# Performance work log

Hardware: AMD Instinct MI355X
Metric: run time of the kernel (lower is better)

The kernel has to match this reference:

```python
import jax, jax.numpy as jnp
import numpy as np

BS, C, N, L = 2, 64, 400, 12   # [bs, c, N, L]
D, H = 128, 8                  # model_dim, num_heads
HD = D // H                    # head_dim = 16
FF = 1024                      # feed_forward_dim
EPS_LN = 1e-5
EPS_NORM = 1e-12


def setup_inputs() -> dict:
    key = jax.random.key(0)
    ks = jax.random.split(key, 24)
    w = lambda k, shape: jax.random.normal(k, shape, jnp.float32) * 0.02
    inp = {
        "x":     jax.random.normal(ks[0], (BS, C, N, L), jnp.float32),
        "x_au1": jax.random.normal(ks[1], (BS, C, N, L), jnp.float32),
        "x_au2": jax.random.normal(ks[2], (BS, C, N, L), jnp.float32),
        # projections stored as [in, out] so y = x @ W + b
        "WQ1": w(ks[3], (C, D)),  "bQ1": jnp.zeros((D,)),
        "WQ2": w(ks[4], (C, D)),  "bQ2": jnp.zeros((D,)),
        "WK1": w(ks[5], (C, D)),  "bK1": jnp.zeros((D,)),
        "WK2": w(ks[6], (C, D)),  "bK2": jnp.zeros((D,)),
        "WV":  w(ks[7], (C, D)),  "bV":  jnp.zeros((D,)),
        "Wo":  w(ks[8], (D, C)),  "bo":  jnp.zeros((C,)),
        "Wf1": w(ks[9], (C, FF)), "bf1": jnp.zeros((FF,)),
        "Wf2": w(ks[10], (FF, C)),"bf2": jnp.zeros((C,)),
        "g1": jnp.ones((C,)), "be1": jnp.zeros((C,)),
        "g2": jnp.ones((C,)), "be2": jnp.zeros((C,)),
        "temperature": jnp.ones((H,)),
        "alphas": jnp.ones((2,)) / 2.0,
    }
    return inp


def _layernorm(x, g, b):
    m = jnp.mean(x, axis=-1, keepdims=True)
    v = jnp.var(x, axis=-1, keepdims=True)
    return (x - m) * jax.lax.rsqrt(v + EPS_LN) * g + b


def _l2norm(x):
    n = jnp.linalg.norm(x, axis=-1, keepdims=True)
    return x / jnp.maximum(n, EPS_NORM)


def _topk_masked(attn, k):
    # keep entries >= k-th largest along last axis (ties measure-zero for floats)
    kth = jax.lax.top_k(attn, k)[0][..., -1:]
    return jnp.where(attn >= kth, attn, -jnp.inf)


def reference(x, x_au1, x_au2, WQ1, bQ1, WQ2, bQ2, WK1, bK1, WK2, bK2,
              WV, bV, Wo, bo, Wf1, bf1, Wf2, bf2, g1, be1, g2, be2,
              temperature, alphas):
    # [bs,c,N,L] -> [bs,L,N,c]
    xt  = jnp.transpose(x,     (0, 3, 2, 1))
    a1t = jnp.transpose(x_au1, (0, 3, 2, 1))
    a2t = jnp.transpose(x_au2, (0, 3, 2, 1))
    bs, Lq, Nq, c = xt.shape

    def heads(t):  # [bs,L,N,D] -> [bs,L,N,H,hd]
        return t.reshape(bs, Lq, Nq, H, HD)

    q1 = _l2norm(heads(a1t @ WQ1 + bQ1))
    q2 = _l2norm(heads(a2t @ WQ2 + bQ2))
    k1 = _l2norm(heads(xt  @ WK1 + bK1))
    k2 = _l2norm(heads(xt  @ WK2 + bK2))
    v  = heads(xt @ WV + bV)

    # dual cosine attention scores: [bs,H,L,N,N]
    attn = (jnp.einsum('blnhd,blmhd->bhlnm', q1, k1)
            + jnp.einsum('blnhd,blmhd->bhlnm', q2, k2))
    attn = attn * temperature.reshape(1, H, 1, 1, 1)

    k_top1 = max(1, Nq // 2)
    k_top2 = max(1, Nq // 4)
    p1 = jax.nn.softmax(_topk_masked(attn, k_top1), axis=-1)
    p2 = jax.nn.softmax(_topk_masked(attn, k_top2), axis=-1)

    out1 = jnp.einsum('bhlnm,blmhd->blnhd', p1, v)
    out2 = jnp.einsum('bhlnm,blmhd->blnhd', p2, v)
    al = jax.nn.softmax(alphas)
    out = (out1 * al[0] + out2 * al[1]).reshape(bs, Lq, Nq, D)

    out = out @ Wo + bo
    out = _layernorm(xt + out, g1, be1)
    ff = jax.nn.relu(out @ Wf1 + bf1) @ Wf2 + bf2
    out = _layernorm(out + ff, g2, be2)
    out = jnp.transpose(out, (0, 3, 2, 1))  # back to [bs,c,N,L]

    attn_flat = attn.reshape(bs * H, Lq, Nq, Nq)
    p2_flat = p2.reshape(bs * H, Lq, Nq, Nq)
    return out, attn_flat, p2_flat
```

## Files before the change

### kernel.cpp

```cpp
#include <hip/hip_runtime.h>
#include <math.h>

#define BSZ 2
#define CHN 64
#define NPT 400
#define LW  12
#define DM  128
#define NH  8
#define HDM 16
#define FFD 1024
#define NTOK (BSZ*LW*NPT)

#define TA 16
__global__ __launch_bounds__(128) void stage_a(
    const float* __restrict__ x, const float* __restrict__ xa1, const float* __restrict__ xa2,
    const float* __restrict__ WQ1, const float* __restrict__ bQ1,
    const float* __restrict__ WQ2, const float* __restrict__ bQ2,
    const float* __restrict__ WK1, const float* __restrict__ bK1,
    const float* __restrict__ WK2, const float* __restrict__ bK2,
    const float* __restrict__ WV,  const float* __restrict__ bV,
    float* __restrict__ q1n, float* __restrict__ q2n,
    float* __restrict__ k1n, float* __restrict__ k2n, float* __restrict__ vv)
{
  __shared__ float xv[TA][CHN], a1v[TA][CHN], a2v[TA][CHN];
  const int tid = threadIdx.x;
  const int t0 = blockIdx.x * TA;
  for (int i = tid; i < TA*CHN; i += 128) {
    int tt = i & (TA-1), c = i >> 4;
    int token = t0 + tt;
    int n = token % NPT; int bl = token / NPT; int l = bl % LW; int b = bl / LW;
    int gidx = ((b*CHN + c)*NPT + n)*LW + l;
    xv[tt][c] = x[gidx]; a1v[tt][c] = xa1[gidx]; a2v[tt][c] = xa2[gidx];
  }
  __syncthreads();
  const int d = tid;
  float aq1[TA], aq2[TA], ak1[TA], ak2[TA], av[TA];
  float b1 = bQ1[d], b2 = bQ2[d], b3 = bK1[d], b4 = bK2[d], b5 = bV[d];
  #pragma unroll
  for (int t = 0; t < TA; ++t) { aq1[t]=b1; aq2[t]=b2; ak1[t]=b3; ak2[t]=b4; av[t]=b5; }
  for (int c = 0; c < CHN; ++c) {
    float w1 = WQ1[c*DM + d], w2 = WQ2[c*DM + d], w3 = WK1[c*DM + d],
          w4 = WK2[c*DM + d], w5 = WV[c*DM + d];
    #pragma unroll
    for (int t = 0; t < TA; ++t) {
      float xc = xv[t][c], x1 = a1v[t][c], x2 = a2v[t][c];
      aq1[t] += x1*w1; aq2[t] += x2*w2; ak1[t] += xc*w3; ak2[t] += xc*w4; av[t] += xc*w5;
    }
  }
  const int h = d >> 4, dd = d & 15;
  #pragma unroll
  for (int t = 0; t < TA; ++t) {
    float s1 = aq1[t]*aq1[t], s2 = aq2[t]*aq2[t], s3 = ak1[t]*ak1[t], s4 = ak2[t]*ak2[t];
    #pragma unroll
    for (int m = 1; m < 16; m <<= 1) {
      s1 += __shfl_xor(s1, m); s2 += __shfl_xor(s2, m);
      s3 += __shfl_xor(s3, m); s4 += __shfl_xor(s4, m);
    }
    float i1 = 1.f/fmaxf(sqrtf(s1),1e-12f), i2 = 1.f/fmaxf(sqrtf(s2),1e-12f),
          i3 = 1.f/fmaxf(sqrtf(s3),1e-12f), i4 = 1.f/fmaxf(sqrtf(s4),1e-12f);
    int token = t0 + t;
    int n = token % NPT; int bl = token / NPT; int l = bl % LW; int b = bl / LW;
    int base = (((b*LW + l)*NH + h)*NPT + n)*HDM + dd;
    q1n[base] = aq1[t]*i1; q2n[base] = aq2[t]*i2;
    k1n[base] = ak1[t]*i3; k2n[base] = ak2[t]*i4; vv[base] = av[t];
  }
}

__device__ __forceinline__ unsigned okey(float xf) {
  unsigned u = __float_as_uint(xf);
  return (u & 0x80000000u) ? ~u : (u | 0x80000000u);
}

__global__ __launch_bounds__(256, 2) void stage_b(
    const float* __restrict__ q1n, const float* __restrict__ q2n,
    const float* __restrict__ k1n, const float* __restrict__ k2n,
    const float* __restrict__ vv,
    const float* __restrict__ temperature, const float* __restrict__ alphas,
    float* __restrict__ attn_o, float* __restrict__ p2_o, float* __restrict__ oa)
{
  __shared__ float4 k1s[4*401], k2s[4*401], vs[4*401];
  int wg = blockIdx.x;
  const int s = wg & 3; wg >>= 2;
  const int l = wg % LW; wg /= LW;
  const int h = wg & 7; const int b = wg >> 3;
  const int tid = threadIdx.x, lane = tid & 63, wave = tid >> 6;

  const int slice = (b*LW + l)*NH + h;
  const int oslice = (b*NH + h)*LW + l;
  const float4* k1g = (const float4*)(k1n + slice*NPT*HDM);
  const float4* k2g = (const float4*)(k2n + slice*NPT*HDM);
  const float4* vg  = (const float4*)(vv  + slice*NPT*HDM);
  for (int i = tid; i < NPT*4; i += 256) {
    int m = i >> 2, w4 = i & 3;
    k1s[w4*401 + m] = k1g[i];
    k2s[w4*401 + m] = k2g[i];
    vs [w4*401 + m] = vg[i];
  }
  __syncthreads();

  const float temp = temperature[h];
  float a0 = alphas[0], a1 = alphas[1];
  float amx = fmaxf(a0, a1);
  float e0 = __expf(a0 - amx), e1 = __expf(a1 - amx);
  float al0 = e0/(e0+e1), al1 = e1/(e0+e1);

  const float* q1base = q1n + slice*NPT*HDM;
  const float* q2base = q2n + slice*NPT*HDM;
  float* attn_base = attn_o + (size_t)oslice*NPT*NPT;
  float* p2_base   = p2_o   + (size_t)oslice*NPT*NPT;
  const int tokbase = (b*LW + l)*NPT;

  for (int bi = wave; bi < 25; bi += 4) {
    const int nb = s*100 + bi*4;
    float sc[4][7];
    #pragma unroll
    for (int r = 0; r < 4; ++r)
      #pragma unroll
      for (int j = 0; j < 7; ++j) sc[r][j] = 0.f;

    #pragma unroll
    for (int ch = 0; ch < 4; ++ch) {
      float4 q1c[4], q2c[4];
      #pragma unroll
      for (int r = 0; r < 4; ++r) {
        q1c[r] = *(const float4*)(q1base + (nb+r)*HDM + ch*4);
        q2c[r] = *(const float4*)(q2base + (nb+r)*HDM + ch*4);
      }
      #pragma unroll
      for (int j = 0; j < 7; ++j) {
        int m = lane + 64*j;
        if (j < 6 || lane < 16) {
          float4 kc1 = k1s[ch*401 + m];
          float4 kc2 = k2s[ch*401 + m];
          #pragma unroll
          for (int r = 0; r < 4; ++r) {
            sc[r][j] += q1c[r].x*kc1.x + q1c[r].y*kc1.y + q1c[r].z*kc1.z + q1c[r].w*kc1.w
                      + q2c[r].x*kc2.x + q2c[r].y*kc2.y + q2c[r].z*kc2.z + q2c[r].w*kc2.w;
          }
        }
      }
    }
    #pragma unroll
    for (int r = 0; r < 4; ++r) {
      #pragma unroll
      for (int j = 0; j < 7; ++j) {
        sc[r][j] *= temp;
        int m = lane + 64*j;
        if (j < 6 || lane < 16)
          __builtin_nontemporal_store(sc[r][j], &attn_base[(nb + r)*NPT + m]);
      }
    }
    #pragma unroll
    for (int r = 0; r < 4; ++r) {
      unsigned key[7];
      #pragma unroll
      for (int j = 0; j < 7; ++j) {
        bool valid = (j < 6) || (lane < 16);
        key[j] = valid ? okey(sc[r][j]) : 0u;
      }
      float am = -3.4e38f;
      #pragma unroll
      for (int j = 0; j < 7; ++j) if ((j < 6) || (lane < 16)) am = fmaxf(am, sc[r][j]);
      #pragma unroll
      for (int m2 = 1; m2 < 64; m2 <<= 1) am = fmaxf(am, __shfl_xor(am, m2));

      unsigned v1 = 0u, v2 = 0u;
      bool d1 = false, d2 = false;
      #pragma clang loop unroll(disable)
      for (int bit = 31; bit >= 0; --bit) {
        if (!d1) {
          unsigned T1 = v1 | (1u << bit);
          int c1 = 0;
          #pragma unroll
          for (int j = 0; j < 7; ++j) c1 += __popcll(__ballot(key[j] >= T1));
          if (c1 >= 200) { v1 = T1; if (c1 == 200) d1 = true; }
        }
        if (!d2) {
          unsigned T2 = v2 | (1u << bit);
          int c2 = 0;
          #pragma unroll
          for (int j = 0; j < 7; ++j) c2 += __popcll(__ballot(key[j] >= T2));
          if (c2 >= 100) { v2 = T2; if (c2 == 100) d2 = true; }
        }
        if (d1 && d2) break;
      }

      float e[7]; float s1 = 0.f, s2 = 0.f;
      #pragma unroll
      for (int j = 0; j < 7; ++j) {
        e[j] = ((j < 6) || (lane < 16)) ? __expf(sc[r][j] - am) : 0.f;
        s1 += (key[j] >= v1) ? e[j] : 0.f;
        s2 += (key[j] >= v2) ? e[j] : 0.f;
      }
      #pragma unroll
      for (int m2 = 1; m2 < 64; m2 <<= 1) { s1 += __shfl_xor(s1, m2); s2 += __shfl_xor(s2, m2); }
      float rz1 = 1.f / s1, rz2 = 1.f / s2;
      float c1 = al0 * rz1, c2 = al1 * rz2;
      #pragma unroll
      for (int j = 0; j < 7; ++j) {
        int m = lane + 64*j;
        float p2v = (key[j] >= v2) ? e[j]*rz2 : 0.f;
        if ((j < 6) || (lane < 16))
          __builtin_nontemporal_store(p2v, &p2_base[(nb + r)*NPT + m]);
        sc[r][j] = e[j] * (((key[j] >= v1) ? c1 : 0.f) + ((key[j] >= v2) ? c2 : 0.f));
      }
    }
    #pragma unroll
    for (int half = 0; half < 2; ++half) {
      float buf[32];
      #pragma unroll
      for (int i = 0; i < 32; ++i) buf[i] = 0.f;
      #pragma unroll
      for (int j = 0; j < 7; ++j) {
        int m = lane + 64*j;
        if (j < 6 || lane < 16) {
          float4 w0 = vs[(half*2+0)*401 + m];
          float4 w1 = vs[(half*2+1)*401 + m];
          #pragma unroll
          for (int r = 0; r < 4; ++r) {
            float wr = sc[r][j];
            buf[r*8+0] += wr*w0.x; buf[r*8+1] += wr*w0.y;
            buf[r*8+2] += wr*w0.z; buf[r*8+3] += wr*w0.w;
            buf[r*8+4] += wr*w1.x; buf[r*8+5] += wr*w1.y;
            buf[r*8+6] += wr*w1.z; buf[r*8+7] += wr*w1.w;
          }
        }
      }
      #pragma unroll
      for (int st = 0; st < 5; ++st) {
        int bsel = (lane >> st) & 1;
        #pragma unroll
        for (int u = 0; u < (32 >> (st+1)); ++u) {
          float lo = buf[2*u], hi = buf[2*u+1];
          float keep = bsel ? hi : lo;
          float send = bsel ? lo : hi;
          float recv = __shfl_xor(send, 1 << st);
          buf[u] = keep + recv;
        }
      }
      float res = buf[0] + __shfl_xor(buf[0], 32);
      if (lane < 32) {
        int rr = lane >> 3, dlo = lane & 7;
        oa[(tokbase + nb + rr)*DM + h*HDM + half*8 + dlo] = res;
      }
    }
  }
}

#define TC 32
__global__ __launch_bounds__(256, 2) void stage_c(
    const float* __restrict__ oa, const float* __restrict__ x,
    const float* __restrict__ Wo, const float* __restrict__ bo,
    const float* __restrict__ Wf1, const float* __restrict__ bf1,
    const float* __restrict__ Wf2, const float* __restrict__ bf2,
    const float* __restrict__ g1, const float* __restrict__ be1,
    const float* __restrict__ g2, const float* __restrict__ be2,
    float* __restrict__ outp)
{
  __shared__ float4 oa_lds[TC*32];
  __shared__ float4 y1_lds[TC*16];
  __shared__ float4 act_lds[TC*64];
  const int tid = threadIdx.x;
  const int t0 = blockIdx.x * TC;
  const float4* oag = (const float4*)(oa + t0*DM);
  for (int i = tid; i < TC*32; i += 256) oa_lds[i] = oag[i];
  __syncthreads();

  const int c = tid & 63, g = tid >> 6;
  float bo_c = bo[c], g1c = g1[c], be1c = be1[c], g2c = g2[c], be2c = be2[c], bf2c = bf2[c];

  float o1[8];
  #pragma unroll
  for (int k = 0; k < 8; ++k) o1[k] = bo_c;
  for (int d4 = 0; d4 < 32; ++d4) {
    float w0 = Wo[(4*d4+0)*CHN + c];
    float w1 = Wo[(4*d4+1)*CHN + c];
    float w2 = Wo[(4*d4+2)*CHN + c];
    float w3 = Wo[(4*d4+3)*CHN + c];
    #pragma unroll
    for (int k = 0; k < 8; ++k) {
      float4 u = oa_lds[(g + 4*k)*32 + d4];
      o1[k] += u.x*w0 + u.y*w1 + u.z*w2 + u.w*w3;
    }
  }
  float y1r[8];
  #pragma unroll
  for (int k = 0; k < 8; ++k) {
    int token = t0 + g + 4*k;
    int n = token % NPT; int bl = token / NPT; int l = bl % LW; int b = bl / LW;
    float val = o1[k] + x[((b*CHN + c)*NPT + n)*LW + l];
    float sm = val, sq = val*val;
    #pragma unroll
    for (int m2 = 1; m2 < 64; m2 <<= 1) { sm += __shfl_xor(sm, m2); sq += __shfl_xor(sq, m2); }
    float mean = sm * (1.f/64.f);
    float var = sq * (1.f/64.f) - mean*mean;
    float y = (val - mean) * rsqrtf(var + 1e-5f) * g1c + be1c;
    y1r[k] = y;
    ((float*)y1_lds)[(g + 4*k)*CHN + c] = y;
  }
  __syncthreads();

  float o2a[8];
  #pragma unroll
  for (int k = 0; k < 8; ++k) o2a[k] = 0.f;

  for (int fb = 0; fb < 4; ++fb) {
    {
      const int ft = tid & 63, ga = tid >> 6;
      const int f = fb*256 + ft*4;
      float4 facc[8];
      float4 bb = *(const float4*)(bf1 + f);
      #pragma unroll
      for (int k = 0; k < 8; ++k) facc[k] = bb;
      for (int c4 = 0; c4 < 16; ++c4) {
        float4 w0 = *(const float4*)(Wf1 + (4*c4+0)*FFD + f);
        float4 w1 = *(const float4*)(Wf1 + (4*c4+1)*FFD + f);
        float4 w2 = *(const float4*)(Wf1 + (4*c4+2)*FFD + f);
        float4 w3 = *(const float4*)(Wf1 + (4*c4+3)*FFD + f);
        #pragma unroll
        for (int k = 0; k < 8; ++k) {
          float4 y4 = y1_lds[(ga + 4*k)*16 + c4];
          facc[k].x += y4.x*w0.x + y4.y*w1.x + y4.z*w2.x + y4.w*w3.x;
          facc[k].y += y4.x*w0.y + y4.y*w1.y + y4.z*w2.y + y4.w*w3.y;
          facc[k].z += y4.x*w0.z + y4.y*w1.z + y4.z*w2.z + y4.w*w3.z;
          facc[k].w += y4.x*w0.w + y4.y*w1.w + y4.z*w2.w + y4.w*w3.w;
        }
      }
      #pragma unroll
      for (int k = 0; k < 8; ++k) {
        float4 rv;
        rv.x = fmaxf(facc[k].x, 0.f); rv.y = fmaxf(facc[k].y, 0.f);
        rv.z = fmaxf(facc[k].z, 0.f); rv.w = fmaxf(facc[k].w, 0.f);
        act_lds[(ga + 4*k)*64 + ft] = rv;
      }
    }
    __syncthreads();
    for (int f4 = 0; f4 < 64; ++f4) {
      int f = fb*256 + f4*4;
      float w0 = Wf2[(f+0)*CHN + c];
      float w1 = Wf2[(f+1)*CHN + c];
      float w2 = Wf2[(f+2)*CHN + c];
      float w3 = Wf2[(f+3)*CHN + c];
      #pragma unroll
      for (int k = 0; k < 8; ++k) {
        float4 a4 = act_lds[(g + 4*k)*64 + f4];
        o2a[k] += a4.x*w0 + a4.y*w1 + a4.z*w2 + a4.w*w3;
      }
    }
    __syncthreads();
  }
  #pragma unroll
  for (int k = 0; k < 8; ++k) {
    int token = t0 + g + 4*k;
    int n = token % NPT; int bl = token / NPT; int l = bl % LW; int b = bl / LW;
    float val = y1r[k] + o2a[k] + bf2c;
    float sm = val, sq = val*val;
    #pragma unroll
    for (int m2 = 1; m2 < 64; m2 <<= 1) { sm += __shfl_xor(sm, m2); sq += __shfl_xor(sq, m2); }
    float mean = sm * (1.f/64.f);
    float var = sq * (1.f/64.f) - mean*mean;
    float y = (val - mean) * rsqrtf(var + 1e-5f) * g2c + be2c;
    outp[((b*CHN + c)*NPT + n)*LW + l] = y;
  }
}

extern "C" void kernel_launch(void* const* d_in, const int* in_sizes, int n_in,
                              void* d_out, int out_size, void* d_ws, size_t ws_size,
                              hipStream_t stream) {
  const float* x    = (const float*)d_in[0];
  const float* xa1  = (const float*)d_in[1];
  const float* xa2  = (const float*)d_in[2];
  const float* WQ1  = (const float*)d_in[3];
  const float* bQ1  = (const float*)d_in[4];
  const float* WQ2  = (const float*)d_in[5];
  const float* bQ2  = (const float*)d_in[6];
  const float* WK1  = (const float*)d_in[7];
  const float* bK1  = (const float*)d_in[8];
  const float* WK2  = (const float*)d_in[9];
  const float* bK2  = (const float*)d_in[10];
  const float* WV   = (const float*)d_in[11];
  const float* bV   = (const float*)d_in[12];
  const float* Wo   = (const float*)d_in[13];
  const float* bo   = (const float*)d_in[14];
  const float* Wf1  = (const float*)d_in[15];
  const float* bf1  = (const float*)d_in[16];
  const float* Wf2  = (const float*)d_in[17];
  const float* bf2  = (const float*)d_in[18];
  const float* g1   = (const float*)d_in[19];
  const float* be1  = (const float*)d_in[20];
  const float* g2   = (const float*)d_in[21];
  const float* be2  = (const float*)d_in[22];
  const float* temp = (const float*)d_in[23];
  const float* alph = (const float*)d_in[24];

  float* outp   = (float*)d_out;
  float* attn_o = outp + (size_t)BSZ*CHN*NPT*LW;
  float* p2_o   = attn_o + (size_t)BSZ*NH*LW*NPT*NPT;

  const size_t SLICE = (size_t)BSZ*LW*NH*NPT*HDM;
  float* w   = (float*)d_ws;
  float* q1n = w;             w += SLICE;
  float* q2n = w;             w += SLICE;
  float* k1n = w;             w += SLICE;
  float* k2n = w;             w += SLICE;
  float* vv  = w;             w += SLICE;
  float* oa  = w;             w += (size_t)NTOK*DM;

  stage_a<<<NTOK/TA, 128, 0, stream>>>(x, xa1, xa2, WQ1, bQ1, WQ2, bQ2,
                                       WK1, bK1, WK2, bK2, WV, bV,
                                       q1n, q2n, k1n, k2n, vv);
  stage_b<<<BSZ*NH*LW*4, 256, 0, stream>>>(q1n, q2n, k1n, k2n, vv,
                                           temp, alph, attn_o, p2_o, oa);
  stage_c<<<NTOK/TC, 256, 0, stream>>>(oa, x, Wo, bo, Wf1, bf1, Wf2, bf2,
                                       g1, be1, g2, be2, outp);
}
```

Before: 1.338 ms.

## Split attention rows over more workgroups and interleave per-row top-k bisection

Stage_b now splits each (b,l,h) slice into 8 workgroups instead of 4, using an uneven 13/12 row-group split. This doubles the grid to fill more compute units, at the cost of loading K/V into shared memory twice as often. The radix-bisection top-k threshold search now runs over all 4 rows of a block inside one bit loop, so the serial ballot chains from different rows overlap and there is more instruction-level parallelism. The price is more registers for the key arrays, which could hurt occupancy.

```diff
diff --git a/kernel.cpp b/kernel.cpp
--- a/kernel.cpp
+++ b/kernel.cpp
@@ -10,6 +10,7 @@
 #define HDM 16
 #define FFD 1024
 #define NTOK (BSZ*LW*NPT)
+#define SPLIT 8
 
 #define TA 16
 __global__ __launch_bounds__(128) void stage_a(
@@ -80,10 +81,13 @@
 {
   __shared__ float4 k1s[4*401], k2s[4*401], vs[4*401];
   int wg = blockIdx.x;
-  const int s = wg & 3; wg >>= 2;
+  const int s = wg & (SPLIT-1); wg /= SPLIT;
   const int l = wg % LW; wg /= LW;
   const int h = wg & 7; const int b = wg >> 3;
   const int tid = threadIdx.x, lane = tid & 63, wave = tid >> 6;
+
+  const int g0  = s*12 + (s < 4 ? s : 4);
+  const int cnt = (s < 4) ? 13 : 12;
 
   const int slice = (b*LW + l)*NH + h;
   const int oslice = (b*NH + h)*LW + l;
@@ -110,8 +114,8 @@
   float* p2_base   = p2_o   + (size_t)oslice*NPT*NPT;
   const int tokbase = (b*LW + l)*NPT;
 
-  for (int bi = wave; bi < 25; bi += 4) {
-    const int nb = s*100 + bi*4;
+  for (int bi = wave; bi < cnt; bi += 4) {
+    const int nb = (g0 + bi)*4;
     float sc[4][7];
     #pragma unroll
     for (int r = 0; r < 4; ++r)
@@ -150,47 +154,58 @@
           __builtin_nontemporal_store(sc[r][j], &attn_base[(nb + r)*NPT + m]);
       }
     }
+    unsigned key[4][7];
+    #pragma unroll
+    for (int r = 0; r < 4; ++r)
+      #pragma unroll
+      for (int j = 0; j < 7; ++j) {
+        bool valid = (j < 6) || (lane < 16);
+        key[r][j] = valid ? okey(sc[r][j]) : 0u;
+      }
+    float am[4];
     #pragma unroll
     for (int r = 0; r < 4; ++r) {
-      unsigned key[7];
-      #pragma unroll
-      for (int j = 0; j < 7; ++j) {
-        bool valid = (j < 6) || (lane < 16);
-        key[j] = valid ? okey(sc[r][j]) : 0u;
-      }
-      float am = -3.4e38f;
-      #pragma unroll
-      for (int j = 0; j < 7; ++j) if ((j < 6) || (lane < 16)) am = fmaxf(am, sc[r][j]);
-      #pragma unroll
-      for (int m2 = 1; m2 < 64; m2 <<= 1) am = fmaxf(am, __shfl_xor(am, m2));
-
-      unsigned v1 = 0u, v2 = 0u;
-      bool d1 = false, d2 = false;
-      #pragma clang loop unroll(disable)
-      for (int bit = 31; bit >= 0; --bit) {
-        if (!d1) {
-          unsigned T1 = v1 | (1u << bit);
-          int c1 = 0;
+      float a = -3.4e38f;
+      #pragma unroll
+      for (int j = 0; j < 7; ++j) if ((j < 6) || (lane < 16)) a = fmaxf(a, sc[r][j]);
+      am[r] = a;
+    }
+    #pragma unroll
+    for (int m2 = 1; m2 < 64; m2 <<= 1) {
+      #pragma unroll
+      for (int r = 0; r < 4; ++r) am[r] = fmaxf(am[r], __shfl_xor(am[r], m2));
+    }
+    unsigned v1[4] = {0u,0u,0u,0u}, v2[4] = {0u,0u,0u,0u};
+    unsigned done = 0u;
+    #pragma clang loop unroll(disable)
+    for (int bit = 31; bit >= 0; --bit) {
+      #pragma unroll
+      for (int r = 0; r < 4; ++r) {
+        if (!(done & (1u << r))) {
+          unsigned T = v1[r] | (1u << bit);
+          int c = 0;
           #pragma unroll
-          for (int j = 0; j < 7; ++j) c1 += __popcll(__ballot(key[j] >= T1));
-          if (c1 >= 200) { v1 = T1; if (c1 == 200) d1 = true; }
-        }
-        if (!d2) {
-          unsigned T2 = v2 | (1u << bit);
-          int c2 = 0;
+          for (int j = 0; j < 7; ++j) c += __popcll(__ballot(key[r][j] >= T));
+          if (c >= 200) { v1[r] = T; if (c == 200) done |= (1u << r); }
+        }
+        if (!(done & (16u << r))) {
+          unsigned T = v2[r] | (1u << bit);
+          int c = 0;
           #pragma unroll
-          for (int j = 0; j < 7; ++j) c2 += __popcll(__ballot(key[j] >= T2));
-          if (c2 >= 100) { v2 = T2; if (c2 == 100) d2 = true; }
-        }
-        if (d1 && d2) break;
-      }
-
+          for (int j = 0; j < 7; ++j) c += __popcll(__ballot(key[r][j] >= T));
+          if (c >= 100) { v2[r] = T; if (c == 100) done |= (16u << r); }
+        }
+      }
+      if (done == 0xFFu) break;
+    }
+    #pragma unroll
+    for (int r = 0; r < 4; ++r) {
       float e[7]; float s1 = 0.f, s2 = 0.f;
       #pragma unroll
       for (int j = 0; j < 7; ++j) {
-        e[j] = ((j < 6) || (lane < 16)) ? __expf(sc[r][j] - am) : 0.f;
-        s1 += (key[j] >= v1) ? e[j] : 0.f;
-        s2 += (key[j] >= v2) ? e[j] : 0.f;
+        e[j] = ((j < 6) || (lane < 16)) ? __expf(sc[r][j] - am[r]) : 0.f;
+        s1 += (key[r][j] >= v1[r]) ? e[j] : 0.f;
+        s2 += (key[r][j] >= v2[r]) ? e[j] : 0.f;
       }
       #pragma unroll
       for (int m2 = 1; m2 < 64; m2 <<= 1) { s1 += __shfl_xor(s1, m2); s2 += __shfl_xor(s2, m2); }
@@ -199,10 +214,10 @@
       #pragma unroll
       for (int j = 0; j < 7; ++j) {
         int m = lane + 64*j;
-        float p2v = (key[j] >= v2) ? e[j]*rz2 : 0.f;
+        float p2v = (key[r][j] >= v2[r]) ? e[j]*rz2 : 0.f;
         if ((j < 6) || (lane < 16))
           __builtin_nontemporal_store(p2v, &p2_base[(nb + r)*NPT + m]);
-        sc[r][j] = e[j] * (((key[j] >= v1) ? c1 : 0.f) + ((key[j] >= v2) ? c2 : 0.f));
+        sc[r][j] = e[j] * (((key[r][j] >= v1[r]) ? c1 : 0.f) + ((key[r][j] >= v2[r]) ? c2 : 0.f));
       }
     }
     #pragma unroll
@@ -409,8 +424,8 @@
   stage_a<<<NTOK/TA, 128, 0, stream>>>(x, xa1, xa2, WQ1, bQ1, WQ2, bQ2,
                                        WK1, bK1, WK2, bK2, WV, bV,
                                        q1n, q2n, k1n, k2n, vv);
-  stage_b<<<BSZ*NH*LW*4, 256, 0, stream>>>(q1n, q2n, k1n, k2n, vv,
-                                           temp, alph, attn_o, p2_o, oa);
+  stage_b<<<BSZ*NH*LW*SPLIT, 256, 0, stream>>>(q1n, q2n, k1n, k2n, vv,
+                                               temp, alph, attn_o, p2_o, oa);
   stage_c<<<NTOK/TC, 256, 0, stream>>>(oa, x, Wo, bo, Wf1, bf1, Wf2, bf2,
                                        g1, be1, g2, be2, outp);
 }
```

Measured after the change: 1.211 ms. 1.11x faster.
